# Kernel optimization log

Hardware: AMD Instinct MI355X
Metric: run time of the kernel (lower is better)

Reference implementation:

```python
import jax, jax.numpy as jnp
import numpy as np

B, C, W, H = 4, 256, 64, 64
DK = 32


def setup_inputs() -> dict:
    key = jax.random.key(0)
    ks = jax.random.split(key, 5)
    x = jax.random.normal(ks[0], (B, C, W, H), dtype=jnp.float32)
    # 1x1 conv weights ~ linear projections; scale like conv default init
    s = 1.0 / np.sqrt(C)
    Wq = jax.random.normal(ks[1], (DK, C), dtype=jnp.float32) * s
    Wk = jax.random.normal(ks[2], (DK, C), dtype=jnp.float32) * s
    Wv = jax.random.normal(ks[3], (C, C), dtype=jnp.float32) * s
    bq = jnp.zeros((DK,), jnp.float32)
    bk = jnp.zeros((DK,), jnp.float32)
    bv = jnp.zeros((C,), jnp.float32)
    # NOTE: module initializes gamma=0 (output == x, zero grads to Q/K/V);
    # use a nonzero value so the attention path is exercised.
    gamma = jax.random.uniform(ks[4], (1,), dtype=jnp.float32) + 0.5
    return {"x": x, "Wq": Wq, "bq": bq, "Wk": Wk, "bk": bk,
            "Wv": Wv, "bv": bv, "gamma": gamma}


def reference(x, Wq, bq, Wk, bk, Wv, bv, gamma):
    b, c, w, h = x.shape
    n = w * h
    xf = x.reshape(b, c, n)                      # [B, C, N]
    q = jnp.einsum('kc,bcn->bkn', Wq, xf) + bq[None, :, None]  # [B, dk, N]
    k = jnp.einsum('kc,bcn->bkn', Wk, xf) + bk[None, :, None]  # [B, dk, N]
    v = jnp.einsum('oc,bcn->bon', Wv, xf) + bv[None, :, None]  # [B, C, N]
    energy = jnp.einsum('bkn,bkm->bnm', q, k)    # [B, N, N] (no 1/sqrt(dk) scale)
    attn = jax.nn.softmax(energy, axis=-1)       # softmax over keys m
    # out[b,c,n] = sum_m v[b,c,m] * attn[b,n,m]  (bmm(V, A^T))
    out = jnp.einsum('bcm,bnm->bcn', v, attn)
    out = out.reshape(b, c, w, h)
    out = gamma[0] * out + x                      # channel_in == channel_out
    return out
```

## Files before the change

kernel.cpp:

```cpp
#include <hip/hip_runtime.h>
#include <hip/hip_bf16.h>
#include <stdint.h>

typedef float f32x16 __attribute__((ext_vector_type(16)));
typedef short bf16x8 __attribute__((ext_vector_type(8)));

#define L2E 1.4426950408889634f
#define ROWPAT(r, hi) (((r) & 3) + 8 * ((r) >> 2) + 4 * (hi))

#define WCATB_OFF 0u
#define QBUF_OFF  163840u
#define KBUF_OFF  1212416u
#define VBUF_OFF  2260992u

static __device__ __forceinline__ ushort f2bf(float f) {
    union { float f; uint32_t u; } v; v.f = f;
    uint32_t u = v.u;
    return (ushort)((u + 0x7fffu + ((u >> 16) & 1u)) >> 16);
}

static __device__ __forceinline__ uint32_t cvtpk(float lo, float hi) {
    uint32_t r;
    asm volatile("v_cvt_pk_bf16_f32 %0, %1, %2" : "=v"(r) : "v"(lo), "v"(hi));
    return r;
}
static __device__ __forceinline__ bf16x8 packP(float p0, float p1, float p2, float p3,
                                               float p4, float p5, float p6, float p7) {
    uint32_t a0 = cvtpk(p0, p1), a1 = cvtpk(p2, p3);
    uint32_t b0 = cvtpk(p4, p5), b1 = cvtpk(p6, p7);
    auto s0 = __builtin_amdgcn_permlane32_swap(a0, b0, false, false);
    auto s1 = __builtin_amdgcn_permlane32_swap(a1, b1, false, false);
    union { uint32_t u[4]; bf16x8 v; } pk;
    pk.u[0] = s0[0];
    pk.u[1] = s1[0];
    pk.u[2] = s0[1];
    pk.u[3] = s1[1];
    return pk.v;
}

__global__ void prep_kernel(const float* __restrict__ Wq, const float* __restrict__ Wk,
                            const float* __restrict__ Wv, ushort* __restrict__ Wcb) {
    int row = blockIdx.x, c = threadIdx.x;
    float v;
    if (row < 32)      v = Wq[row * 256 + c];
    else if (row < 64) v = Wk[(row - 32) * 256 + c];
    else               v = Wv[(row - 64) * 256 + c];
    Wcb[row * 256 + c] = f2bf(v);
}

__global__ __launch_bounds__(256)
void fproj_kernel(const float* __restrict__ x, const ushort* __restrict__ Wcb,
                  const float* __restrict__ bq, const float* __restrict__ bk,
                  const float* __restrict__ bv,
                  ushort* __restrict__ qbuf, ushort* __restrict__ kbuf,
                  ushort* __restrict__ vbuf) {
    __shared__ ushort xt[32 * 264];
    const int tid = threadIdx.x;
    const int b = blockIdx.x >> 7;
    const int n0 = (blockIdx.x & 127) << 5;

    const float* xb = x + (((size_t)b) << 20) + n0;
    #pragma unroll
    for (int i = 0; i < 8; ++i) {
        int task = tid + (i << 8);
        int c = task >> 3, seg = task & 7;
        float4 v = *(const float4*)(xb + (size_t)c * 4096 + seg * 4);
        xt[(seg * 4 + 0) * 264 + c] = f2bf(v.x);
        xt[(seg * 4 + 1) * 264 + c] = f2bf(v.y);
        xt[(seg * 4 + 2) * 264 + c] = f2bf(v.z);
        xt[(seg * 4 + 3) * 264 + c] = f2bf(v.w);
    }
    __syncthreads();

    const int w = tid >> 6, l = tid & 63;
    const int l31 = l & 31, hi = l >> 5;

    for (int cc = w; cc < 10; cc += 4) {
        const int wbase = (cc < 2) ? cc * 32 : (cc - 2) * 32 + 64;
        const ushort* wrow = Wcb + (size_t)(wbase + l31) * 256;
        f32x16 acc = (f32x16)0.0f;
        if (cc < 2) {
            #pragma unroll
            for (int kk = 0; kk < 16; ++kk) {
                bf16x8 xf = *(const bf16x8*)&xt[l31 * 264 + kk * 16 + hi * 8];
                bf16x8 wf = *(const bf16x8*)&wrow[kk * 16 + hi * 8];
                acc = __builtin_amdgcn_mfma_f32_32x32x16_bf16(xf, wf, acc, 0, 0, 0);
            }
            const float bias = (cc == 0) ? bq[l31] : bk[l31];
            const float scale = (cc == 0) ? L2E : 1.0f;
            ushort* dst = (cc == 0) ? qbuf : kbuf;
            #pragma unroll
            for (int r = 0; r < 16; ++r) {
                int n = n0 + ROWPAT(r, hi);
                dst[((size_t)((b << 12) + n)) * 32 + l31] = f2bf((acc[r] + bias) * scale);
            }
        } else {
            #pragma unroll
            for (int kk = 0; kk < 16; ++kk) {
                bf16x8 wf = *(const bf16x8*)&wrow[kk * 16 + hi * 8];
                bf16x8 xf = *(const bf16x8*)&xt[l31 * 264 + kk * 16 + hi * 8];
                acc = __builtin_amdgcn_mfma_f32_32x32x16_bf16(wf, xf, acc, 0, 0, 0);
            }
            #pragma unroll
            for (int r = 0; r < 16; ++r) {
                int c = (wbase - 64) + ROWPAT(r, hi);
                vbuf[((size_t)(b * 256 + c)) * 4096 + n0 + l31] = f2bf(acc[r] + bv[c]);
            }
        }
    }
}

#define KSTR 36
#define VSTR 66
__global__ __launch_bounds__(256, 2)
void attn_kernel(const ushort* __restrict__ qbuf, const ushort* __restrict__ kbuf,
                 const ushort* __restrict__ vbuf, const float* __restrict__ x,
                 const float* __restrict__ gammap, float* __restrict__ out) {
    __shared__ ushort klds[2][64 * KSTR];
    __shared__ ushort vlds[2][256 * VSTR];
    __shared__ float  dlds[2][32];

    const int tid = threadIdx.x;
    const int bid = blockIdx.x;
    const int work = (bid & 7) * 64 + (bid >> 3);
    const int b = work >> 7;
    const int qbase = (work & 127) << 5;
    const int w = tid >> 6, l = tid & 63;
    const int l31 = l & 31, hi = l >> 5;
    const int kh = w >> 1, cp = w & 1;

    const ushort* kb = kbuf + ((size_t)b << 12) * 32;
    const ushort* vb = vbuf + ((size_t)b << 8) * 4096;

    const ushort* qrow = qbuf + ((size_t)((b << 12) + qbase + l31)) * 32;
    const bf16x8 qf0 = *(const bf16x8*)&qrow[hi * 8];
    const bf16x8 qf1 = *(const bf16x8*)&qrow[16 + hi * 8];

    f32x16 acc[4];
    #pragma unroll
    for (int ch = 0; ch < 4; ++ch) acc[ch] = (f32x16)0.0f;
    float dsum = 0.f;

    const int vc = tid >> 3, vs = tid & 7;
    const int krow = tid >> 2, kseg = tid & 3;
    const ushort* vsrc = vb + (size_t)vc * 4096 + vs * 8;
    const ushort* ksrc = kb + (size_t)krow * 32 + kseg * 8;
    uint4 vreg[8], kreg;

    const int krow_a = (kh * 32 + l31) * KSTR;

    bf16x8 pA0, pA1, pB0, pB1;
    bf16x8 vA0, vA1, vA2, vA3, vA4, vA5, vA6, vA7;
    bf16x8 vB0, vB1, vB2, vB3, vB4, vB5, vB6, vB7;

#define QK_EXP_LOAD(CUR, PC0, PC1, VC0, VC1, VC2, VC3, VC4, VC5, VC6, VC7)     \
    {                                                                          \
        bf16x8 kf0 = *(const bf16x8*)&klds[CUR][krow_a + hi * 8];              \
        bf16x8 kf1 = *(const bf16x8*)&klds[CUR][krow_a + 16 + hi * 8];         \
        f32x16 sT = __builtin_amdgcn_mfma_f32_32x32x16_bf16(kf0, qf0,          \
                                                    (f32x16)0.0f, 0, 0, 0);    \
        sT = __builtin_amdgcn_mfma_f32_32x32x16_bf16(kf1, qf1, sT, 0, 0, 0);   \
        float p[16];                                                           \
        _Pragma("unroll")                                                      \
        for (int r = 0; r < 16; ++r) {                                         \
            p[r] = __builtin_amdgcn_exp2f(sT[r]);                              \
            dsum += p[r];                                                      \
        }                                                                      \
        PC0 = packP(p[0], p[1], p[2], p[3], p[4], p[5], p[6], p[7]);           \
        PC1 = packP(p[8], p[9], p[10], p[11], p[12], p[13], p[14], p[15]);     \
        const int cr0 = (cp * 128 + 0 * 32 + l31) * VSTR + kh * 32;            \
        const int cr1 = (cp * 128 + 1 * 32 + l31) * VSTR + kh * 32;            \
        const int cr2 = (cp * 128 + 2 * 32 + l31) * VSTR + kh * 32;            \
        const int cr3 = (cp * 128 + 3 * 32 + l31) * VSTR + kh * 32;            \
        VC0 = *(const bf16x8*)&vlds[CUR][cr0 + hi * 8];                        \
        VC1 = *(const bf16x8*)&vlds[CUR][cr0 + 16 + hi * 8];                   \
        VC2 = *(const bf16x8*)&vlds[CUR][cr1 + hi * 8];                        \
        VC3 = *(const bf16x8*)&vlds[CUR][cr1 + 16 + hi * 8];                   \
        VC4 = *(const bf16x8*)&vlds[CUR][cr2 + hi * 8];                        \
        VC5 = *(const bf16x8*)&vlds[CUR][cr2 + 16 + hi * 8];                   \
        VC6 = *(const bf16x8*)&vlds[CUR][cr3 + hi * 8];                        \
        VC7 = *(const bf16x8*)&vlds[CUR][cr3 + 16 + hi * 8];                   \
    }

#define PV_OTHER(PO0, PO1, VO0, VO1, VO2, VO3, VO4, VO5, VO6, VO7)             \
    {                                                                          \
        __builtin_amdgcn_s_setprio(1);                                         \
        acc[0] = __builtin_amdgcn_mfma_f32_32x32x16_bf16(VO0, PO0, acc[0], 0, 0, 0); \
        acc[0] = __builtin_amdgcn_mfma_f32_32x32x16_bf16(VO1, PO1, acc[0], 0, 0, 0); \
        acc[1] = __builtin_amdgcn_mfma_f32_32x32x16_bf16(VO2, PO0, acc[1], 0, 0, 0); \
        acc[1] = __builtin_amdgcn_mfma_f32_32x32x16_bf16(VO3, PO1, acc[1], 0, 0, 0); \
        acc[2] = __builtin_amdgcn_mfma_f32_32x32x16_bf16(VO4, PO0, acc[2], 0, 0, 0); \
        acc[2] = __builtin_amdgcn_mfma_f32_32x32x16_bf16(VO5, PO1, acc[2], 0, 0, 0); \
        acc[3] = __builtin_amdgcn_mfma_f32_32x32x16_bf16(VO6, PO0, acc[3], 0, 0, 0); \
        acc[3] = __builtin_amdgcn_mfma_f32_32x32x16_bf16(VO7, PO1, acc[3], 0, 0, 0); \
        __builtin_amdgcn_s_setprio(0);                                         \
    }

#define PREFETCH(KNEXT)                                                        \
    {                                                                          \
        const size_t m0 = (size_t)(KNEXT) << 6;                                \
        _Pragma("unroll")                                                      \
        for (int i = 0; i < 8; ++i)                                            \
            vreg[i] = *(const uint4*)(vsrc + (size_t)i * 32 * 4096 + m0);      \
        kreg = *(const uint4*)(ksrc + (m0 << 5));                              \
    }

#define STAGE_WRITE(DSTBUF)                                                    \
    {                                                                          \
        _Pragma("unroll")                                                      \
        for (int i = 0; i < 8; ++i)                                            \
            *(uint4*)&vlds[DSTBUF][(vc + 32 * i) * VSTR + vs * 8] = vreg[i];   \
        *(uint4*)&klds[DSTBUF][krow * KSTR + kseg * 8] = kreg;                 \
    }

    PREFETCH(0);
    STAGE_WRITE(0);
    __syncthreads();
    PREFETCH(1);
    QK_EXP_LOAD(0, pA0, pA1, vA0, vA1, vA2, vA3, vA4, vA5, vA6, vA7);
    STAGE_WRITE(1);
    __syncthreads();

    for (int k = 1; k < 62; k += 2) {
        PREFETCH(k + 1);
        QK_EXP_LOAD(1, pB0, pB1, vB0, vB1, vB2, vB3, vB4, vB5, vB6, vB7);
        PV_OTHER(pA0, pA1, vA0, vA1, vA2, vA3, vA4, vA5, vA6, vA7);
        STAGE_WRITE(0);
        __syncthreads();
        PREFETCH(k + 2);
        QK_EXP_LOAD(0, pA0, pA1, vA0, vA1, vA2, vA3, vA4, vA5, vA6, vA7);
        PV_OTHER(pB0, pB1, vB0, vB1, vB2, vB3, vB4, vB5, vB6, vB7);
        STAGE_WRITE(1);
        __syncthreads();
    }
    QK_EXP_LOAD(1, pB0, pB1, vB0, vB1, vB2, vB3, vB4, vB5, vB6, vB7);
    PV_OTHER(pA0, pA1, vA0, vA1, vA2, vA3, vA4, vA5, vA6, vA7);
    PV_OTHER(pB0, pB1, vB0, vB1, vB2, vB3, vB4, vB5, vB6, vB7);

#undef QK_EXP_LOAD
#undef PV_OTHER
#undef PREFETCH
#undef STAGE_WRITE

    const float gam = gammap[0];
    float dall = dsum + __shfl_xor(dsum, 32);
    float* scr = (float*)&vlds[0][0];
    __syncthreads();
    if (kh == 1) {
        #pragma unroll
        for (int ch = 0; ch < 4; ++ch)
            #pragma unroll
            for (int r = 0; r < 16; ++r)
                scr[(((cp * 4 + ch) * 16 + r) << 6) + l] = acc[ch][r];
    }
    if (cp == 0 && l < 32) dlds[kh][l31] = dall;
    __syncthreads();
    if (kh == 0) {
        const float denom = dlds[0][l31] + dlds[1][l31];
        const float ginv = gam / denom;
        const float* xb2 = x + (((size_t)b) << 8) * 4096;
        float* ob = out + (((size_t)b) << 8) * 4096;
        const int q = qbase + l31;
        #pragma unroll
        for (int ch = 0; ch < 4; ++ch) {
            #pragma unroll
            for (int r = 0; r < 16; ++r) {
                int c = cp * 128 + ch * 32 + ROWPAT(r, hi);
                float o = acc[ch][r] + scr[(((cp * 4 + ch) * 16 + r) << 6) + l];
                size_t idx = (size_t)c * 4096 + q;
                ob[idx] = o * ginv + xb2[idx];
            }
        }
    }
}

extern "C" void kernel_launch(void* const* d_in, const int* in_sizes, int n_in,
                              void* d_out, int out_size, void* d_ws, size_t ws_size,
                              hipStream_t stream) {
    (void)in_sizes; (void)n_in; (void)out_size; (void)ws_size;
    const float* x     = (const float*)d_in[0];
    const float* Wq    = (const float*)d_in[1];
    const float* bq    = (const float*)d_in[2];
    const float* Wk    = (const float*)d_in[3];
    const float* bk    = (const float*)d_in[4];
    const float* Wv    = (const float*)d_in[5];
    const float* bv    = (const float*)d_in[6];
    const float* gamma = (const float*)d_in[7];
    float* out = (float*)d_out;

    char* ws = (char*)d_ws;
    ushort* Wcb  = (ushort*)(ws + WCATB_OFF);
    ushort* qbuf = (ushort*)(ws + QBUF_OFF);
    ushort* kbuf = (ushort*)(ws + KBUF_OFF);
    ushort* vbuf = (ushort*)(ws + VBUF_OFF);

    prep_kernel<<<320, 256, 0, stream>>>(Wq, Wk, Wv, Wcb);
    fproj_kernel<<<512, 256, 0, stream>>>(x, Wcb, bq, bk, bv, qbuf, kbuf, vbuf);
    attn_kernel<<<512, 256, 0, stream>>>(qbuf, kbuf, vbuf, x, gamma, out);
}
```

Before: 105.5 us.

## Deepen global prefetch to two tiles ahead using alternating register sets

The single register staging buffer for V/K tiles becomes two sets (A and B), so global loads are issued two iterations ahead of their LDS write instead of one. The goal is to hide more global/HBM latency behind the QK-exp and PV MFMA work. In exchange, each thread holds roughly 36 more VGPRs, which may lower occupancy or cause spills. Prefetches past the last tile are clamped to tile 63, which adds redundant loads at the tail.

```diff
diff --git a/kernel.cpp b/kernel.cpp
--- a/kernel.cpp
+++ b/kernel.cpp
@@ -145,7 +145,8 @@
     const int krow = tid >> 2, kseg = tid & 3;
     const ushort* vsrc = vb + (size_t)vc * 4096 + vs * 8;
     const ushort* ksrc = kb + (size_t)krow * 32 + kseg * 8;
-    uint4 vreg[8], kreg;
+    uint4 vregA[8], kregA;
+    uint4 vregB[8], kregB;
 
     const int krow_a = (kh * 32 + l31) * KSTR;
 
@@ -196,42 +197,64 @@
         __builtin_amdgcn_s_setprio(0);                                         \
     }
 
-#define PREFETCH(KNEXT)                                                        \
-    {                                                                          \
-        const size_t m0 = (size_t)(KNEXT) << 6;                                \
+#define PREFETCH_A(KT)                                                         \
+    {                                                                          \
+        const size_t m0 = (size_t)(KT) << 6;                                   \
         _Pragma("unroll")                                                      \
         for (int i = 0; i < 8; ++i)                                            \
-            vreg[i] = *(const uint4*)(vsrc + (size_t)i * 32 * 4096 + m0);      \
-        kreg = *(const uint4*)(ksrc + (m0 << 5));                              \
-    }
-
-#define STAGE_WRITE(DSTBUF)                                                    \
-    {                                                                          \
+            vregA[i] = *(const uint4*)(vsrc + (size_t)i * 32 * 4096 + m0);     \
+        kregA = *(const uint4*)(ksrc + (m0 << 5));                             \
+    }
+#define PREFETCH_B(KT)                                                         \
+    {                                                                          \
+        const size_t m0 = (size_t)(KT) << 6;                                   \
         _Pragma("unroll")                                                      \
         for (int i = 0; i < 8; ++i)                                            \
-            *(uint4*)&vlds[DSTBUF][(vc + 32 * i) * VSTR + vs * 8] = vreg[i];   \
-        *(uint4*)&klds[DSTBUF][krow * KSTR + kseg * 8] = kreg;                 \
-    }
-
-    PREFETCH(0);
-    STAGE_WRITE(0);
-    __syncthreads();
-    PREFETCH(1);
+            vregB[i] = *(const uint4*)(vsrc + (size_t)i * 32 * 4096 + m0);     \
+        kregB = *(const uint4*)(ksrc + (m0 << 5));                             \
+    }
+#define WRITE_A(DSTBUF)                                                        \
+    {                                                                          \
+        _Pragma("unroll")                                                      \
+        for (int i = 0; i < 8; ++i)                                            \
+            *(uint4*)&vlds[DSTBUF][(vc + 32 * i) * VSTR + vs * 8] = vregA[i];  \
+        *(uint4*)&klds[DSTBUF][krow * KSTR + kseg * 8] = kregA;                \
+    }
+#define WRITE_B(DSTBUF)                                                        \
+    {                                                                          \
+        _Pragma("unroll")                                                      \
+        for (int i = 0; i < 8; ++i)                                            \
+            *(uint4*)&vlds[DSTBUF][(vc + 32 * i) * VSTR + vs * 8] = vregB[i];  \
+        *(uint4*)&klds[DSTBUF][krow * KSTR + kseg * 8] = kregB;                \
+    }
+
+    PREFETCH_A(0);
+    WRITE_A(0);
+    __syncthreads();
+    PREFETCH_A(1);
+    PREFETCH_B(2);
     QK_EXP_LOAD(0, pA0, pA1, vA0, vA1, vA2, vA3, vA4, vA5, vA6, vA7);
-    STAGE_WRITE(1);
-    __syncthreads();
+    WRITE_A(1);
+    __syncthreads();
+    PREFETCH_A(3);
 
     for (int k = 1; k < 62; k += 2) {
-        PREFETCH(k + 1);
         QK_EXP_LOAD(1, pB0, pB1, vB0, vB1, vB2, vB3, vB4, vB5, vB6, vB7);
         PV_OTHER(pA0, pA1, vA0, vA1, vA2, vA3, vA4, vA5, vA6, vA7);
-        STAGE_WRITE(0);
+        WRITE_B(0);
         __syncthreads();
-        PREFETCH(k + 2);
+        {
+            const int t = (k + 3 < 63) ? (k + 3) : 63;
+            PREFETCH_B(t);
+        }
         QK_EXP_LOAD(0, pA0, pA1, vA0, vA1, vA2, vA3, vA4, vA5, vA6, vA7);
         PV_OTHER(pB0, pB1, vB0, vB1, vB2, vB3, vB4, vB5, vB6, vB7);
-        STAGE_WRITE(1);
+        WRITE_A(1);
         __syncthreads();
+        {
+            const int t = (k + 4 < 63) ? (k + 4) : 63;
+            PREFETCH_A(t);
+        }
     }
     QK_EXP_LOAD(1, pB0, pB1, vB0, vB1, vB2, vB3, vB4, vB5, vB6, vB7);
     PV_OTHER(pA0, pA1, vA0, vA1, vA2, vA3, vA4, vA5, vA6, vA7);
@@ -239,8 +262,10 @@
 
 #undef QK_EXP_LOAD
 #undef PV_OTHER
-#undef PREFETCH
-#undef STAGE_WRITE
+#undef PREFETCH_A
+#undef PREFETCH_B
+#undef WRITE_A
+#undef WRITE_B
 
     const float gam = gammap[0];
     float dall = dsum + __shfl_xor(dsum, 32);
```

Result: slower. 310.1 us (+194.0%).
